# Kernel tuning notes

Measured on AMD Instinct MI355X. Metric: run time of the kernel, lower is better.

## Reference

```python
import jax, jax.numpy as jnp
import numpy as np

MAX_IN = 1024
MAX_OUT = 4096
LOW_RANK = 64
N_ARCH = 16
HYP_HID = 128


def setup_inputs() -> dict:
    key = jax.random.key(0)
    ks = jax.random.split(key, 9)
    x = jax.random.normal(ks[0], (4, 2048, MAX_IN), dtype=jnp.float32)
    active_arch_embed = jax.random.uniform(ks[1], (N_ARCH,), dtype=jnp.float32)
    # base linear params (PyTorch layout: weight [out, in])
    base_weight = jax.random.normal(ks[2], (MAX_OUT, MAX_IN), dtype=jnp.float32) * 0.02
    base_bias = jax.random.normal(ks[3], (MAX_OUT,), dtype=jnp.float32) * 0.02
    # low rank factor [low_rank, in], init std 0.01 per source
    lr_factor = jax.random.normal(ks[4], (LOW_RANK, MAX_IN), dtype=jnp.float32) * 0.01
    # hypernet: Linear(N_ARCH->HYP_HID), ReLU, Linear(HYP_HID->MAX_OUT*LOW_RANK)
    hyp_w1 = jax.random.normal(ks[5], (HYP_HID, N_ARCH), dtype=jnp.float32) * 0.05
    hyp_b1 = jax.random.normal(ks[6], (HYP_HID,), dtype=jnp.float32) * 0.05
    hyp_w2 = jax.random.normal(ks[7], (MAX_OUT * LOW_RANK, HYP_HID), dtype=jnp.float32) * 0.01
    hyp_b2 = jax.random.normal(ks[8], (MAX_OUT * LOW_RANK,), dtype=jnp.float32) * 0.01
    return {
        'x': x,
        'active_arch_embed': active_arch_embed,
        'base_weight': base_weight,
        'base_bias': base_bias,
        'lr_factor': lr_factor,
        'hyp_w1': hyp_w1,
        'hyp_b1': hyp_b1,
        'hyp_w2': hyp_w2,
        'hyp_b2': hyp_b2,
    }


def reference(x, active_arch_embed, base_weight, base_bias, lr_factor,
              hyp_w1, hyp_b1, hyp_w2, hyp_b2):
    # hypernet MLP on the arch embedding -> low-rank left factor [MAX_OUT, LOW_RANK]
    h = jax.nn.relu(hyp_w1 @ active_arch_embed + hyp_b1)          # [HYP_HID]
    left = (hyp_w2 @ h + hyp_b2).reshape(MAX_OUT, LOW_RANK)        # [out, r]
    # full weight = base + low-rank update (as in source, before slicing)
    weight = base_weight + left @ lr_factor                        # [out, in]
    # active_out = max_out, active_in = x.shape[-1] = max_in -> no slicing
    # F.linear: y = x @ weight.T + bias
    return jnp.einsum('bsi,oi->bso', x, weight) + base_bias
```

## Files before the change

kernel.cpp:

```cpp
#include <hip/hip_runtime.h>

#define MAX_IN   1024
#define MAX_OUT  4096
#define LOW_RANK 64
#define N_ARCH   16
#define HYP_HID  128
#define BATCH_M  8192

typedef __attribute__((ext_vector_type(8))) short short8;
typedef __attribute__((ext_vector_type(4))) float f32x4;

__device__ __forceinline__ unsigned short f2bf(float f) {
  union { float f; unsigned int u; } c; c.f = f;
  unsigned int r = c.u + 0x7fffu + ((c.u >> 16) & 1u);
  return (unsigned short)(r >> 16);
}

__device__ __forceinline__ void gload16(const unsigned short* g, unsigned short* l) {
  __builtin_amdgcn_global_load_lds(
      (const __attribute__((address_space(1))) unsigned int*)(g),
      (__attribute__((address_space(3))) unsigned int*)(l), 16, 0, 0);
}

__global__ __launch_bounds__(256) void convert_x(const float* __restrict__ in,
                                                 unsigned short* __restrict__ out) {
  size_t i = (size_t)blockIdx.x * 256 + threadIdx.x;
  float4 v = *(const float4*)(in + i * 4);
  ushort4 o;
  o.x = f2bf(v.x); o.y = f2bf(v.y); o.z = f2bf(v.z); o.w = f2bf(v.w);
  *(ushort4*)(out + i * 4) = o;
}

__global__ __launch_bounds__(256) void build_w_fused(
    const float* __restrict__ w1, const float* __restrict__ b1,
    const float* __restrict__ e,
    const float* __restrict__ hyp_w2, const float* __restrict__ hyp_b2,
    const float* __restrict__ base_w, const float* __restrict__ lrf,
    unsigned short* __restrict__ Wbf) {
  __shared__ float hs[HYP_HID];
  __shared__ float lefts[8 * LOW_RANK];
  const int tid = threadIdx.x;
  const int o0 = blockIdx.x * 8;

  if (tid < HYP_HID) {
    const float4* wr = (const float4*)(w1 + tid * N_ARCH);
    float s = b1[tid];
#pragma unroll
    for (int c = 0; c < 4; c++) {
      float4 wv = wr[c];
      float4 ev = *(const float4*)(e + c * 4);
      s += wv.x * ev.x + wv.y * ev.y + wv.z * ev.z + wv.w * ev.w;
    }
    hs[tid] = fmaxf(s, 0.0f);
  }
  __syncthreads();

  const int lane = tid & 63;
  const int w = tid >> 6;
  const int g = lane >> 3, gl = lane & 7;
  float4 hf[4];
#pragma unroll
  for (int c = 0; c < 4; c++) hf[c] = *(const float4*)(hs + c * 32 + gl * 4);
#pragma unroll 4
  for (int it = 0; it < 16; ++it) {
    const int rl = w * 128 + it * 8 + g;
    const float* rp = hyp_w2 + (size_t)(o0 * LOW_RANK + rl) * HYP_HID;
    float s = 0.f;
#pragma unroll
    for (int c = 0; c < 4; c++) {
      float4 v = *(const float4*)(rp + c * 32 + gl * 4);
      s += v.x * hf[c].x + v.y * hf[c].y + v.z * hf[c].z + v.w * hf[c].w;
    }
    s += __shfl_xor(s, 4);
    s += __shfl_xor(s, 2);
    s += __shfl_xor(s, 1);
    if (gl == 0) lefts[rl] = s + hyp_b2[o0 * LOW_RANK + rl];
  }
  __syncthreads();

#pragma unroll
  for (int kk = 0; kk < 4; kk++) {
    const int k = kk * 256 + tid;
    float acc[8];
#pragma unroll
    for (int oi = 0; oi < 8; oi++) acc[oi] = base_w[(size_t)(o0 + oi) * MAX_IN + k];
    for (int r = 0; r < LOW_RANK; r++) {
      float lv = lrf[r * MAX_IN + k];
#pragma unroll
      for (int oi = 0; oi < 8; oi++) acc[oi] += lefts[oi * LOW_RANK + r] * lv;
    }
#pragma unroll
    for (int oi = 0; oi < 8; oi++)
      Wbf[(size_t)(o0 + oi) * MAX_IN + k] = f2bf(acc[oi]);
  }
}

__global__ __launch_bounds__(512, 2) void gemm_kernel(
    const unsigned short* __restrict__ A,
    const unsigned short* __restrict__ B,
    const float* __restrict__ bias,
    float* __restrict__ C) {
  constexpr int K = MAX_IN;
  constexpr int N = MAX_OUT;
  constexpr int SLOT = 32768;
  constexpr int BOFF = 16384;
  constexpr int NT = K / 64;
  __shared__ __align__(16) unsigned short lds[2 * SLOT];

  const int tid = threadIdx.x;
  const int lane = tid & 63;
  const int w = tid >> 6;
  const int wm = w >> 2, wn = w & 3;
  const int fl = lane & 15, hi = lane >> 4;

  const int orig = blockIdx.x;
  const int macro = orig & 7;
  const int mj = orig >> 3;
  const int bm = ((macro >> 1) * 8 + (mj >> 3)) * 256;
  const int bn = ((macro & 1) * 8 + (mj & 7)) * 256;

  const int rid = tid >> 3;
  const int cst = (tid & 7) ^ (rid & 7);
  const unsigned short* Asrc = A + (size_t)(bm + rid) * K + cst * 8;
  const unsigned short* Bsrc = B + (size_t)(bn + rid) * K + cst * 8;

  const int swk0 = (hi ^ (fl & 7)) * 8;
  const int swk1 = ((4 + hi) ^ (fl & 7)) * 8;
  const int arow = (wm * 128 + fl) * 64;
  const int brow = (wn * 64 + fl) * 64;

  f32x4 acc[8][4];
#pragma unroll
  for (int m = 0; m < 8; m++)
#pragma unroll
    for (int n = 0; n < 4; n++) acc[m][n] = (f32x4){0.f, 0.f, 0.f, 0.f};

  short8 a[4][2], b0[2][2], b1[2][2];

#define STAGE_A(s, h, kt)                                                      \
  do {                                                                         \
    gload16(Asrc + (size_t)((h) * 128) * K + (kt) * 64,                        \
            &lds[(s) * SLOT + (((h) * 2) * 512 + tid) * 8]);                   \
    gload16(Asrc + (size_t)((h) * 128 + 64) * K + (kt) * 64,                   \
            &lds[(s) * SLOT + (((h) * 2 + 1) * 512 + tid) * 8]);               \
  } while (0)
#define STAGE_B(s, h, kt)                                                      \
  do {                                                                         \
    gload16(Bsrc + (size_t)((h) * 128) * K + (kt) * 64,                        \
            &lds[(s) * SLOT + BOFF + (((h) * 2) * 512 + tid) * 8]);            \
    gload16(Bsrc + (size_t)((h) * 128 + 64) * K + (kt) * 64,                   \
            &lds[(s) * SLOT + BOFF + (((h) * 2 + 1) * 512 + tid) * 8]);        \
  } while (0)
#define LDA(qm)                                                                \
  _Pragma("unroll") for (int m = 0; m < 4; m++) {                              \
    a[m][0] = *(const short8*)&Aslot[arow + (qm) * 4096 + m * 1024 + swk0];    \
    a[m][1] = *(const short8*)&Aslot[arow + (qm) * 4096 + m * 1024 + swk1];    \
  }
#define LDB(dst, qn)                                                           \
  _Pragma("unroll") for (int n = 0; n < 2; n++) {                              \
    dst[n][0] = *(const short8*)&Bslot[brow + (qn) * 2048 + n * 1024 + swk0];  \
    dst[n][1] = *(const short8*)&Bslot[brow + (qn) * 2048 + n * 1024 + swk1];  \
  }
#define MFMA16(qm, qn, bb)                                                     \
  __builtin_amdgcn_s_setprio(1);                                               \
  _Pragma("unroll") for (int m = 0; m < 4; m++)                                \
  _Pragma("unroll") for (int n = 0; n < 2; n++)                                \
  _Pragma("unroll") for (int kk = 0; kk < 2; kk++)                             \
    acc[(qm) * 4 + m][(qn) * 2 + n] = __builtin_amdgcn_mfma_f32_16x16x32_bf16( \
        a[m][kk], bb[n][kk], acc[(qm) * 4 + m][(qn) * 2 + n], 0, 0, 0);        \
  __builtin_amdgcn_s_setprio(0);
#define BAR1() __builtin_amdgcn_s_barrier();                                   \
  asm volatile("s_waitcnt lgkmcnt(0)" ::: "memory");                           \
  __builtin_amdgcn_sched_barrier(0)
#define BAR2() __builtin_amdgcn_s_barrier(); __builtin_amdgcn_sched_barrier(0)

  STAGE_A(0, 0, 0); STAGE_A(0, 1, 0);
  STAGE_B(0, 0, 0); STAGE_B(0, 1, 0);
  STAGE_B(1, 0, 1); STAGE_B(1, 1, 1);
  asm volatile("s_waitcnt vmcnt(4)" ::: "memory");
  __builtin_amdgcn_s_barrier();
  __builtin_amdgcn_sched_barrier(0);

  for (int t = 0; t < NT; ++t) {
    const unsigned short* Aslot = &lds[(t & 1) * SLOT];
    const unsigned short* Bslot = Aslot + BOFF;
    LDA(0); LDB(b0, 0);
    if (t + 1 < NT) STAGE_A((t + 1) & 1, 0, t + 1);
    BAR1();
    MFMA16(0, 0, b0);
    BAR2();
    LDB(b1, 1);
    if (t + 1 < NT) STAGE_A((t + 1) & 1, 1, t + 1);
    BAR1();
    MFMA16(0, 1, b1);
    BAR2();
    LDA(1);
    if (t + 2 < NT) STAGE_B(t & 1, 0, t + 2);
    BAR1();
    MFMA16(1, 1, b1);
    BAR2();
    if (t + 2 < NT) STAGE_B(t & 1, 1, t + 2);
    __builtin_amdgcn_s_barrier();
    __builtin_amdgcn_sched_barrier(0);
    MFMA16(1, 0, b0);
    if (t + 2 < NT) {
      asm volatile("s_waitcnt vmcnt(4)" ::: "memory");
    } else if (t + 1 < NT) {
      asm volatile("s_waitcnt vmcnt(0)" ::: "memory");
    }
    if (t + 1 < NT) { BAR2(); }
  }
#undef STAGE_A
#undef STAGE_B
#undef LDA
#undef LDB
#undef MFMA16
#undef BAR1
#undef BAR2

  float bv[4];
#pragma unroll
  for (int n = 0; n < 4; n++) bv[n] = bias[bn + wn * 64 + n * 16 + fl];
#pragma unroll
  for (int m = 0; m < 8; m++) {
    const int gr0 = bm + wm * 128 + m * 16 + hi * 4;
#pragma unroll
    for (int n = 0; n < 4; n++) {
      const int gc = bn + wn * 64 + n * 16 + fl;
#pragma unroll
      for (int jj = 0; jj < 4; jj++)
        C[(size_t)(gr0 + jj) * N + gc] = acc[m][n][jj] + bv[n];
    }
  }
}

extern "C" void kernel_launch(void* const* d_in, const int* in_sizes, int n_in,
                              void* d_out, int out_size, void* d_ws, size_t ws_size,
                              hipStream_t stream) {
  const float* x      = (const float*)d_in[0];
  const float* embed  = (const float*)d_in[1];
  const float* base_w = (const float*)d_in[2];
  const float* base_b = (const float*)d_in[3];
  const float* lrf    = (const float*)d_in[4];
  const float* w1     = (const float*)d_in[5];
  const float* b1     = (const float*)d_in[6];
  const float* w2     = (const float*)d_in[7];
  const float* b2     = (const float*)d_in[8];
  float* out = (float*)d_out;

  char* ws = (char*)d_ws;
  unsigned short* Xbf = (unsigned short*)ws;
  unsigned short* Wbf = (unsigned short*)(ws + (size_t)BATCH_M * MAX_IN * 2);

  hipLaunchKernelGGL(convert_x, dim3(BATCH_M * MAX_IN / 1024), dim3(256), 0, stream, x, Xbf);
  hipLaunchKernelGGL(build_w_fused, dim3(MAX_OUT / 8), dim3(256), 0, stream,
                     w1, b1, embed, w2, b2, base_w, lrf, Wbf);
  hipLaunchKernelGGL(gemm_kernel, dim3((BATCH_M / 256) * (MAX_OUT / 256)), dim3(512), 0, stream,
                     Xbf, Wbf, base_b, out);
}
```

Baseline: 150.3 us.

## Split hypernet build into its own kernel and make GEMM blocks compute two N-tiles

The fused weight builder is split in two. build_left spreads the hyp_w2 GEMV over many more blocks, and build_w only forms the low-rank update plus base weight. The GEMM grid shrinks from 512 to 256 blocks, and each block runs two consecutive 256-wide N tiles with the same A rows, re-running the prologue and epilogue between them. This aims to raise parallelism in the hypernet stage and to fit the GEMM into a single wave on the CUs. The trade-off is an extra launch and a pipeline drain and refill between the two tiles, and left is stored in the output buffer when the workspace is too small.

Result: slower. 172.1 us (+14.4%).

```diff
diff --git a/kernel.cpp b/kernel.cpp
--- a/kernel.cpp
+++ b/kernel.cpp
@@ -31,17 +31,13 @@
   *(ushort4*)(out + i * 4) = o;
 }
 
-__global__ __launch_bounds__(256) void build_w_fused(
+__global__ __launch_bounds__(256) void build_left(
     const float* __restrict__ w1, const float* __restrict__ b1,
     const float* __restrict__ e,
     const float* __restrict__ hyp_w2, const float* __restrict__ hyp_b2,
-    const float* __restrict__ base_w, const float* __restrict__ lrf,
-    unsigned short* __restrict__ Wbf) {
+    float* __restrict__ left) {
   __shared__ float hs[HYP_HID];
-  __shared__ float lefts[8 * LOW_RANK];
   const int tid = threadIdx.x;
-  const int o0 = blockIdx.x * 8;
-
   if (tid < HYP_HID) {
     const float4* wr = (const float4*)(w1 + tid * N_ARCH);
     float s = b1[tid];
@@ -56,15 +52,17 @@
   __syncthreads();
 
   const int lane = tid & 63;
-  const int w = tid >> 6;
-  const int g = lane >> 3, gl = lane & 7;
+  const int g = lane >> 3;
+  const int gl = lane & 7;
   float4 hf[4];
 #pragma unroll
-  for (int c = 0; c < 4; c++) hf[c] = *(const float4*)(hs + c * 32 + gl * 4);
-#pragma unroll 4
-  for (int it = 0; it < 16; ++it) {
-    const int rl = w * 128 + it * 8 + g;
-    const float* rp = hyp_w2 + (size_t)(o0 * LOW_RANK + rl) * HYP_HID;
+  for (int c = 0; c < 4; c++) hf[c] = *(const float4*)(&hs[c * 32 + gl * 4]);
+  const int wid = blockIdx.x * 4 + (tid >> 6);
+  const int row0 = wid * 32;
+#pragma unroll
+  for (int it = 0; it < 4; it++) {
+    const int row = row0 + it * 8 + g;
+    const float* rp = hyp_w2 + (size_t)row * HYP_HID;
     float s = 0.f;
 #pragma unroll
     for (int c = 0; c < 4; c++) {
@@ -74,8 +72,19 @@
     s += __shfl_xor(s, 4);
     s += __shfl_xor(s, 2);
     s += __shfl_xor(s, 1);
-    if (gl == 0) lefts[rl] = s + hyp_b2[o0 * LOW_RANK + rl];
-  }
+    if (gl == 0) left[row] = s + hyp_b2[row];
+  }
+}
+
+__global__ __launch_bounds__(256) void build_w(
+    const float* __restrict__ left, const float* __restrict__ base_w,
+    const float* __restrict__ lrf, unsigned short* __restrict__ Wbf) {
+  __shared__ float lefts[8 * LOW_RANK];
+  const int tid = threadIdx.x;
+  const int o0 = blockIdx.x * 8;
+#pragma unroll
+  for (int i = tid; i < 8 * LOW_RANK; i += 256)
+    lefts[i] = left[o0 * LOW_RANK + i];
   __syncthreads();
 
 #pragma unroll
@@ -114,10 +123,10 @@
   const int fl = lane & 15, hi = lane >> 4;
 
   const int orig = blockIdx.x;
-  const int macro = orig & 7;
+  const int xcd = orig & 7;
   const int mj = orig >> 3;
-  const int bm = ((macro >> 1) * 8 + (mj >> 3)) * 256;
-  const int bn = ((macro & 1) * 8 + (mj & 7)) * 256;
+  const int bm = ((xcd >> 1) * 8 + (mj >> 2)) * 256;
+  int bn = ((xcd & 1) * 4 + (mj & 3)) * 512;
 
   const int rid = tid >> 3;
   const int cst = (tid & 7) ^ (rid & 7);
@@ -173,42 +182,75 @@
   asm volatile("s_waitcnt lgkmcnt(0)" ::: "memory");                           \
   __builtin_amdgcn_sched_barrier(0)
 #define BAR2() __builtin_amdgcn_s_barrier(); __builtin_amdgcn_sched_barrier(0)
-
-  STAGE_A(0, 0, 0); STAGE_A(0, 1, 0);
-  STAGE_B(0, 0, 0); STAGE_B(0, 1, 0);
-  STAGE_B(1, 0, 1); STAGE_B(1, 1, 1);
-  asm volatile("s_waitcnt vmcnt(4)" ::: "memory");
-  __builtin_amdgcn_s_barrier();
-  __builtin_amdgcn_sched_barrier(0);
-
-  for (int t = 0; t < NT; ++t) {
-    const unsigned short* Aslot = &lds[(t & 1) * SLOT];
-    const unsigned short* Bslot = Aslot + BOFF;
-    LDA(0); LDB(b0, 0);
-    if (t + 1 < NT) STAGE_A((t + 1) & 1, 0, t + 1);
-    BAR1();
-    MFMA16(0, 0, b0);
-    BAR2();
-    LDB(b1, 1);
-    if (t + 1 < NT) STAGE_A((t + 1) & 1, 1, t + 1);
-    BAR1();
-    MFMA16(0, 1, b1);
-    BAR2();
-    LDA(1);
-    if (t + 2 < NT) STAGE_B(t & 1, 0, t + 2);
-    BAR1();
-    MFMA16(1, 1, b1);
-    BAR2();
-    if (t + 2 < NT) STAGE_B(t & 1, 1, t + 2);
-    __builtin_amdgcn_s_barrier();
-    __builtin_amdgcn_sched_barrier(0);
-    MFMA16(1, 0, b0);
-    if (t + 2 < NT) {
-      asm volatile("s_waitcnt vmcnt(4)" ::: "memory");
-    } else if (t + 1 < NT) {
-      asm volatile("s_waitcnt vmcnt(0)" ::: "memory");
-    }
-    if (t + 1 < NT) { BAR2(); }
+#define PROLOGUE()                                                             \
+  do {                                                                         \
+    STAGE_A(0, 0, 0); STAGE_A(0, 1, 0);                                        \
+    STAGE_B(0, 0, 0); STAGE_B(0, 1, 0);                                        \
+    STAGE_B(1, 0, 1); STAGE_B(1, 1, 1);                                        \
+    asm volatile("s_waitcnt vmcnt(4)" ::: "memory");                           \
+    __builtin_amdgcn_s_barrier();                                              \
+    __builtin_amdgcn_sched_barrier(0);                                         \
+  } while (0)
+
+  PROLOGUE();
+
+  for (int tile = 0; tile < 2; ++tile) {
+    for (int t = 0; t < NT; ++t) {
+      const unsigned short* Aslot = &lds[(t & 1) * SLOT];
+      const unsigned short* Bslot = Aslot + BOFF;
+      LDA(0); LDB(b0, 0);
+      if (t + 1 < NT) STAGE_A((t + 1) & 1, 0, t + 1);
+      BAR1();
+      MFMA16(0, 0, b0);
+      BAR2();
+      LDB(b1, 1);
+      if (t + 1 < NT) STAGE_A((t + 1) & 1, 1, t + 1);
+      BAR1();
+      MFMA16(0, 1, b1);
+      BAR2();
+      LDA(1);
+      if (t + 2 < NT) STAGE_B(t & 1, 0, t + 2);
+      BAR1();
+      MFMA16(1, 1, b1);
+      BAR2();
+      if (t + 2 < NT) STAGE_B(t & 1, 1, t + 2);
+      __builtin_amdgcn_s_barrier();
+      __builtin_amdgcn_sched_barrier(0);
+      MFMA16(1, 0, b0);
+      if (t + 2 < NT) {
+        asm volatile("s_waitcnt vmcnt(4)" ::: "memory");
+      } else if (t + 1 < NT) {
+        asm volatile("s_waitcnt vmcnt(0)" ::: "memory");
+      }
+      if (t + 1 < NT) { BAR2(); }
+    }
+
+    {
+      float bv[4];
+#pragma unroll
+      for (int n = 0; n < 4; n++) bv[n] = bias[bn + wn * 64 + n * 16 + fl];
+#pragma unroll
+      for (int m = 0; m < 8; m++) {
+        const int gr0 = bm + wm * 128 + m * 16 + hi * 4;
+#pragma unroll
+        for (int n = 0; n < 4; n++) {
+          const int gc = bn + wn * 64 + n * 16 + fl;
+#pragma unroll
+          for (int jj = 0; jj < 4; jj++)
+            C[(size_t)(gr0 + jj) * N + gc] = acc[m][n][jj] + bv[n];
+        }
+      }
+    }
+
+    if (tile == 0) {
+#pragma unroll
+      for (int m = 0; m < 8; m++)
+#pragma unroll
+        for (int n = 0; n < 4; n++) acc[m][n] = (f32x4){0.f, 0.f, 0.f, 0.f};
+      bn += 256;
+      Bsrc += (size_t)256 * K;
+      PROLOGUE();
+    }
   }
 #undef STAGE_A
 #undef STAGE_B
@@ -217,21 +259,7 @@
 #undef MFMA16
 #undef BAR1
 #undef BAR2
-
-  float bv[4];
-#pragma unroll
-  for (int n = 0; n < 4; n++) bv[n] = bias[bn + wn * 64 + n * 16 + fl];
-#pragma unroll
-  for (int m = 0; m < 8; m++) {
-    const int gr0 = bm + wm * 128 + m * 16 + hi * 4;
-#pragma unroll
-    for (int n = 0; n < 4; n++) {
-      const int gc = bn + wn * 64 + n * 16 + fl;
-#pragma unroll
-      for (int jj = 0; jj < 4; jj++)
-        C[(size_t)(gr0 + jj) * N + gc] = acc[m][n][jj] + bv[n];
-    }
-  }
+#undef PROLOGUE
 }
 
 extern "C" void kernel_launch(void* const* d_in, const int* in_sizes, int n_in,
@@ -250,11 +278,19 @@
 
   char* ws = (char*)d_ws;
   unsigned short* Xbf = (unsigned short*)ws;
-  unsigned short* Wbf = (unsigned short*)(ws + (size_t)BATCH_M * MAX_IN * 2);
+  size_t off_w = (size_t)BATCH_M * MAX_IN * 2;
+  unsigned short* Wbf = (unsigned short*)(ws + off_w);
+  size_t off_left = off_w + (size_t)MAX_OUT * MAX_IN * 2;
+  size_t need = off_left + (size_t)MAX_OUT * LOW_RANK * 4;
+  float* left = (ws_size >= need)
+      ? (float*)(ws + off_left)
+      : out + ((size_t)BATCH_M * MAX_OUT - (size_t)MAX_OUT * LOW_RANK);
 
   hipLaunchKernelGGL(convert_x, dim3(BATCH_M * MAX_IN / 1024), dim3(256), 0, stream, x, Xbf);
-  hipLaunchKernelGGL(build_w_fused, dim3(MAX_OUT / 8), dim3(256), 0, stream,
-                     w1, b1, embed, w2, b2, base_w, lrf, Wbf);
-  hipLaunchKernelGGL(gemm_kernel, dim3((BATCH_M / 256) * (MAX_OUT / 256)), dim3(512), 0, stream,
+  hipLaunchKernelGGL(build_left, dim3(MAX_OUT * LOW_RANK / 128), dim3(256), 0, stream,
+                     w1, b1, embed, w2, b2, left);
+  hipLaunchKernelGGL(build_w, dim3(MAX_OUT / 8), dim3(256), 0, stream,
+                     left, base_w, lrf, Wbf);
+  hipLaunchKernelGGL(gemm_kernel, dim3(256), dim3(512), 0, stream,
                      Xbf, Wbf, base_b, out);
 }
```
